# Kernel tuning notes

Hardware: AMD Instinct MI355X
Metric: run time of the kernel (lower is better)

## Reference

```python
import jax, jax.numpy as jnp
import numpy as np

N = 1_000_000
H = 256
DIMS = [1, H, H, H, H]
N_LAYERS = 4  # 4 linear layers, sin activation after the first 3


def setup_inputs() -> dict:
    key = jax.random.key(0)
    ks = jax.random.split(key, 1 + 2 * N_LAYERS)
    d = {"x": jax.random.normal(ks[0], (N, 2), dtype=jnp.float32)}
    i = 1
    for pre in ("x", "t"):
        for l in range(N_LAYERS):
            lim = 1.0 / np.sqrt(DIMS[l])  # torch.nn.Linear default init range
            d[f"{pre}W{l}"] = jax.random.uniform(
                ks[i], (DIMS[l], DIMS[l + 1]), dtype=jnp.float32, minval=-lim, maxval=lim)
            d[f"{pre}b{l}"] = jnp.zeros((DIMS[l + 1],), dtype=jnp.float32)
            i += 1
    return d


def _mlp(h, params):
    # params: list of (W, b); sin activation after all but the last layer
    n = len(params)
    for idx, (W, b) in enumerate(params):
        h = h @ W + b
        if idx < n - 1:
            h = jnp.sin(h)
    return h


def reference(x, xW0, xb0, xW1, xb1, xW2, xb2, xW3, xb3,
              tW0, tb0, tW1, tb1, tW2, tb2, tW3, tb3):
    x_params = [(xW0, xb0), (xW1, xb1), (xW2, xb2), (xW3, xb3)]
    t_params = [(tW0, tb0), (tW1, tb1), (tW2, tb2), (tW3, tb3)]
    nx = _mlp(x[:, 0:1], x_params)  # [N, H]
    nt = _mlp(x[:, 1:2], t_params)  # [N, H]
    # diag(A @ B.T) == rowwise dot product; avoids the O(N^2) matmul
    even = jnp.sum(nx[:, 0::2] * nt[:, 0::2], axis=-1)  # [N]
    odd = jnp.sum(nx[:, 1::2] * nt[:, 1::2], axis=-1)   # [N]
    return jnp.stack([even, odd], axis=-1)  # [N, 2]
```

## Files before the change

kernel.cpp:

```cpp
#include <hip/hip_runtime.h>


typedef _Float16 f16x8 __attribute__((ext_vector_type(8)));
typedef _Float16 f16x4 __attribute__((ext_vector_type(4)));
typedef float f32x4 __attribute__((ext_vector_type(4)));

__device__ __forceinline__ int hswz(int m, int kbyte) {
    return m * 512 + ((((kbyte >> 4) ^ (m & 7)) & 31) << 4) + (kbyte & 15);
}

__device__ __forceinline__ void barrier_lds() {
    asm volatile("s_waitcnt lgkmcnt(0)" ::: "memory");
    __builtin_amdgcn_s_barrier();
}

__global__ void prepack(const float* __restrict__ xW1, const float* __restrict__ xW2,
                        const float* __restrict__ xW3, const float* __restrict__ tW1,
                        const float* __restrict__ tW2, const float* __restrict__ tW3,
                        _Float16* __restrict__ dst)
{
    int g = blockIdx.x * 256 + threadIdx.x;
    int L = g >> 16;
    int r = g & 65535;
    int j    = r & 7;
    int ln   = (r >> 3) & 15;
    int quad = (r >> 7) & 3;
    int nhi  = (r >> 9) & 15;
    int ks   = (r >> 13) & 1;
    int c    = (r >> 14) & 3;
    const float* W;
    switch (L) {
        case 0: W = xW1; break;
        case 1: W = xW2; break;
        case 2: W = xW3; break;
        case 3: W = tW1; break;
        case 4: W = tW2; break;
        default: W = tW3; break;
    }
    int n = nhi * 16 + ln;
    int k = c * 64 + ks * 32 + quad * 8 + j;
    dst[g] = (_Float16)W[k * 256 + n];
}


__device__ __forceinline__ void layer0_scalar(
    float xv, const float* __restrict__ W0, const float* __restrict__ b0,
    _Float16* __restrict__ hb, int tid)
{
    int m = tid >> 2;
    int q = tid & 3;
#pragma unroll
    for (int g = 0; g < 8; ++g) {
        int n0 = g * 32 + q * 8;
        f16x8 hv;
#pragma unroll
        for (int e = 0; e < 8; ++e) {
            float z = fmaf(xv, W0[n0 + e], b0[n0 + e]);
            hv[e] = (_Float16)__sinf(z);
        }
        *(f16x8*)((char*)hb + hswz(m, n0 * 2)) = hv;
    }
}

template<int MODE>
__device__ __forceinline__ void gemm_phase(
    const _Float16* __restrict__ Wl,
    const _Float16* __restrict__ Wnext,
    const _Float16* __restrict__ rb,
    f32x4 acc[4][4], f16x8 afr[2][4],
    f32x4 wacc[4][4],
    const float* __restrict__ wbias,
    _Float16* __restrict__ wb_lds,
    float xv,
    const float* __restrict__ W0,
    const float* __restrict__ b0,
    int tid, int lane, int ln, int quad, int wave)
{
    f32x4 zero = {0.f, 0.f, 0.f, 0.f};
#pragma unroll
    for (int i = 0; i < 4; ++i)
#pragma unroll
        for (int j = 0; j < 4; ++j)
            acc[i][j] = zero;

    const _Float16* abase = Wl + wave * 2048 + lane * 8;

    f16x8 bfr[2][4];
#pragma unroll
    for (int j = 0; j < 4; ++j)
        bfr[0][j] = *(const f16x8*)((const char*)rb +
                                    hswz(16 * j + ln, quad * 16));

#pragma unroll
    for (int g = 0; g < 8; ++g) {
        if (g < 7) {
#pragma unroll
            for (int j = 0; j < 4; ++j)
                bfr[(g + 1) & 1][j] = *(const f16x8*)((const char*)rb +
                                 hswz(16 * j + ln, (g + 1) * 64 + quad * 16));
        }

        __builtin_amdgcn_s_setprio(1);
#pragma unroll
        for (int i = 0; i < 4; ++i)
#pragma unroll
            for (int j = 0; j < 4; ++j)
                acc[i][j] = __builtin_amdgcn_mfma_f32_16x16x32_f16(
                    afr[g & 1][i], bfr[g & 1][j], acc[i][j], 0, 0, 0);
        __builtin_amdgcn_s_setprio(0);

        if (g < 6) {
#pragma unroll
            for (int i = 0; i < 4; ++i)
                afr[g & 1][i] = *(const f16x8*)(abase + (g + 2) * 8192 + i * 512);
        } else if (Wnext) {
#pragma unroll
            for (int i = 0; i < 4; ++i)
                afr[g & 1][i] = *(const f16x8*)(Wnext + (g - 6) * 8192 +
                                                wave * 2048 + lane * 8 + i * 512);
        }

        if (MODE == 1) {
            const int wi = g >> 1;
            const int nb = wave * 64 + 16 * wi + quad * 4;
            f32x4 bv = *(const f32x4*)&wbias[nb];
#pragma unroll
            for (int jo = 0; jo < 2; ++jo) {
                const int wj = (g & 1) * 2 + jo;
                f16x4 hv;
                hv[0] = (_Float16)__sinf(wacc[wi][wj][0] + bv[0]);
                hv[1] = (_Float16)__sinf(wacc[wi][wj][1] + bv[1]);
                hv[2] = (_Float16)__sinf(wacc[wi][wj][2] + bv[2]);
                hv[3] = (_Float16)__sinf(wacc[wi][wj][3] + bv[3]);
                *(f16x4*)((char*)wb_lds + hswz(16 * wj + ln, nb * 2)) = hv;
            }
        } else if (MODE == 2) {
            const int m = tid >> 2, q = tid & 3;
            const int n0 = g * 32 + q * 8;
            f16x8 hv;
#pragma unroll
            for (int e = 0; e < 8; ++e) {
                float z = fmaf(xv, W0[n0 + e], b0[n0 + e]);
                hv[e] = (_Float16)__sinf(z);
            }
            *(f16x8*)((char*)wb_lds + hswz(m, n0 * 2)) = hv;
        }
    }
}

__global__ __launch_bounds__(256, 2)
void mlp_fused(const float* __restrict__ x,
               const float* __restrict__ xW0, const float* __restrict__ xb0,
               const float* __restrict__ xb1, const float* __restrict__ xb2,
               const float* __restrict__ xb3,
               const float* __restrict__ tW0, const float* __restrict__ tb0,
               const float* __restrict__ tb1, const float* __restrict__ tb2,
               const float* __restrict__ tb3,
               const _Float16* __restrict__ Wp,
               float* __restrict__ out)
{
    __shared__ __align__(16) _Float16 hbuf[2][64 * 256];
    __shared__ __align__(16) float    params[10 * 256];

    const int tid = threadIdx.x;
    const int lane = tid & 63;
    const int wave = tid >> 6;
    const int ln = lane & 15;
    const int quad = lane >> 4;
    const int row0 = blockIdx.x * 64;

    {
        const float* psrc[10] = {xW0, xb0, tW0, tb0, xb1, xb2, xb3, tb1, tb2, tb3};
#pragma unroll
        for (int s = 0; s < 10; ++s)
            params[s * 256 + tid] = psrc[s][tid];
    }
    const float2 xv2 = ((const float2*)x)[row0 + (tid >> 2)];

    f32x4 xacc[4][4], tacc[4][4];
    f16x8 afr[2][4];

#pragma unroll
    for (int s = 0; s < 2; ++s)
#pragma unroll
        for (int i = 0; i < 4; ++i)
            afr[s][i] = *(const f16x8*)(Wp + s * 8192 + wave * 2048 +
                                        lane * 8 + i * 512);
    barrier_lds();

    layer0_scalar(xv2.x, &params[0], &params[256], hbuf[0], tid);
    barrier_lds();

    gemm_phase<2>(Wp + 0 * 65536, Wp + 3 * 65536, hbuf[0], xacc, afr,
                  nullptr, nullptr, hbuf[1],
                  xv2.y, &params[2 * 256], &params[3 * 256],
                  tid, lane, ln, quad, wave);
    barrier_lds();
    gemm_phase<1>(Wp + 3 * 65536, Wp + 1 * 65536, hbuf[1], tacc, afr,
                  xacc, &params[4 * 256], hbuf[0],
                  0.f, nullptr, nullptr, tid, lane, ln, quad, wave);
    barrier_lds();
    gemm_phase<1>(Wp + 1 * 65536, Wp + 4 * 65536, hbuf[0], xacc, afr,
                  tacc, &params[7 * 256], hbuf[1],
                  0.f, nullptr, nullptr, tid, lane, ln, quad, wave);
    barrier_lds();
    gemm_phase<1>(Wp + 4 * 65536, Wp + 2 * 65536, hbuf[1], tacc, afr,
                  xacc, &params[5 * 256], hbuf[0],
                  0.f, nullptr, nullptr, tid, lane, ln, quad, wave);
    barrier_lds();
    gemm_phase<1>(Wp + 2 * 65536, Wp + 5 * 65536, hbuf[0], xacc, afr,
                  tacc, &params[8 * 256], hbuf[1],
                  0.f, nullptr, nullptr, tid, lane, ln, quad, wave);
    barrier_lds();
    gemm_phase<0>(Wp + 5 * 65536, nullptr, hbuf[1], tacc, afr,
                  nullptr, nullptr, nullptr,
                  0.f, nullptr, nullptr, tid, lane, ln, quad, wave);

    const float* xb3l = &params[6 * 256];
    const float* tb3l = &params[9 * 256];
    float ev[4] = {0.f, 0.f, 0.f, 0.f};
    float od[4] = {0.f, 0.f, 0.f, 0.f};
#pragma unroll
    for (int i = 0; i < 4; ++i) {
        int nb = wave * 64 + 16 * i + quad * 4;
        f32x4 xb = *(const f32x4*)&xb3l[nb];
        f32x4 tb = *(const f32x4*)&tb3l[nb];
#pragma unroll
        for (int j = 0; j < 4; ++j) {
            float a0 = xacc[i][j][0] + xb[0], c0 = tacc[i][j][0] + tb[0];
            float a1 = xacc[i][j][1] + xb[1], c1 = tacc[i][j][1] + tb[1];
            float a2 = xacc[i][j][2] + xb[2], c2 = tacc[i][j][2] + tb[2];
            float a3 = xacc[i][j][3] + xb[3], c3 = tacc[i][j][3] + tb[3];
            ev[j] += a0 * c0 + a2 * c2;
            od[j] += a1 * c1 + a3 * c3;
        }
    }
#pragma unroll
    for (int j = 0; j < 4; ++j) {
        ev[j] += __shfl_xor(ev[j], 16, 64);
        ev[j] += __shfl_xor(ev[j], 32, 64);
        od[j] += __shfl_xor(od[j], 16, 64);
        od[j] += __shfl_xor(od[j], 32, 64);
    }

    float* red = (float*)hbuf[0];
    if (lane < 16) {
#pragma unroll
        for (int j = 0; j < 4; ++j) {
            red[wave * 128 + j * 32 + lane * 2 + 0] = ev[j];
            red[wave * 128 + j * 32 + lane * 2 + 1] = od[j];
        }
    }
    __syncthreads();
    if (tid < 128) {
        int jj = tid >> 5, m16 = (tid >> 1) & 15, p = tid & 1;
        int base = jj * 32 + m16 * 2 + p;
        float s = red[base] + red[128 + base] + red[256 + base] + red[384 + base];
        out[(row0 + 16 * jj + m16) * 2 + p] = s;
    }
}

extern "C" void kernel_launch(void* const* d_in, const int* in_sizes, int n_in,
                              void* d_out, int out_size, void* d_ws, size_t ws_size,
                              hipStream_t stream)
{
    const float* x   = (const float*)d_in[0];
    const float* xW0 = (const float*)d_in[1];
    const float* xb0 = (const float*)d_in[2];
    const float* xW1 = (const float*)d_in[3];
    const float* xb1 = (const float*)d_in[4];
    const float* xW2 = (const float*)d_in[5];
    const float* xb2 = (const float*)d_in[6];
    const float* xW3 = (const float*)d_in[7];
    const float* xb3 = (const float*)d_in[8];
    const float* tW0 = (const float*)d_in[9];
    const float* tb0 = (const float*)d_in[10];
    const float* tW1 = (const float*)d_in[11];
    const float* tb1 = (const float*)d_in[12];
    const float* tW2 = (const float*)d_in[13];
    const float* tb2 = (const float*)d_in[14];
    const float* tW3 = (const float*)d_in[15];
    const float* tb3 = (const float*)d_in[16];

    _Float16* Wp = (_Float16*)d_ws;
    const int N = in_sizes[0] / 2;

    prepack<<<1536, 256, 0, stream>>>(xW1, xW2, xW3, tW1, tW2, tW3, Wp);
    mlp_fused<<<N / 64, 256, 0, stream>>>(x, xW0, xb0, xb1, xb2, xb3,
                                          tW0, tb0, tb1, tb2, tb3,
                                          Wp, (float*)d_out);
}
```

Measured before the change: 825.9 us.

## Switch fused MLP GEMMs from 16x16x32 to 32x32x16 MFMA tiles

Replaces the 16x16x32 f16 MFMA tiling with 32x32x16 MFMAs, so each wave holds a 2x2 grid of 32x32 accumulators instead of 4x4 16x16 ones. The weight prepack layout, the LDS swizzle (now XORing with the full row index), the B-fragment prefetch schedule, the sin/bias epilogue write-back and the final row reduction are all rewritten to match the new fragment layout. The larger MFMA shape is meant to cut instruction issue count and LDS B-fragment traffic per FLOP. In exchange it changes register pressure and the bank-conflict pattern of the LDS accesses.

```diff
diff --git a/kernel.cpp b/kernel.cpp
--- a/kernel.cpp
+++ b/kernel.cpp
@@ -4,9 +4,10 @@
 typedef _Float16 f16x8 __attribute__((ext_vector_type(8)));
 typedef _Float16 f16x4 __attribute__((ext_vector_type(4)));
 typedef float f32x4 __attribute__((ext_vector_type(4)));
-
-__device__ __forceinline__ int hswz(int m, int kbyte) {
-    return m * 512 + ((((kbyte >> 4) ^ (m & 7)) & 31) << 4) + (kbyte & 15);
+typedef float f32x16 __attribute__((ext_vector_type(16)));
+
+__device__ __forceinline__ int hswz32(int m, int kbyte) {
+    return m * 512 + ((((kbyte >> 4) ^ m) & 31) << 4) + (kbyte & 15);
 }
 
 __device__ __forceinline__ void barrier_lds() {
@@ -22,12 +23,12 @@
     int g = blockIdx.x * 256 + threadIdx.x;
     int L = g >> 16;
     int r = g & 65535;
-    int j    = r & 7;
-    int ln   = (r >> 3) & 15;
-    int quad = (r >> 7) & 3;
-    int nhi  = (r >> 9) & 15;
-    int ks   = (r >> 13) & 1;
-    int c    = (r >> 14) & 3;
+    int j  = r & 7;
+    int l  = (r >> 3) & 63;
+    int ks = (r >> 9) & 1;
+    int ci = (r >> 10) & 1;
+    int wv = (r >> 11) & 3;
+    int gg = (r >> 13) & 7;
     const float* W;
     switch (L) {
         case 0: W = xW1; break;
@@ -37,8 +38,8 @@
         case 4: W = tW2; break;
         default: W = tW3; break;
     }
-    int n = nhi * 16 + ln;
-    int k = c * 64 + ks * 32 + quad * 8 + j;
+    int n = wv * 64 + ci * 32 + (l & 31);
+    int k = gg * 32 + ks * 16 + ((l >> 5) & 1) * 8 + j;
     dst[g] = (_Float16)W[k * 256 + n];
 }
 
@@ -58,7 +59,7 @@
             float z = fmaf(xv, W0[n0 + e], b0[n0 + e]);
             hv[e] = (_Float16)__sinf(z);
         }
-        *(f16x8*)((char*)hb + hswz(m, n0 * 2)) = hv;
+        *(f16x8*)((char*)hb + hswz32(m, n0 * 2)) = hv;
     }
 }
 
@@ -67,72 +68,85 @@
     const _Float16* __restrict__ Wl,
     const _Float16* __restrict__ Wnext,
     const _Float16* __restrict__ rb,
-    f32x4 acc[4][4], f16x8 afr[2][4],
-    f32x4 wacc[4][4],
+    f32x16 acc[2][2], f16x8 afr[2][4],
+    f32x16 wacc[2][2],
     const float* __restrict__ wbias,
     _Float16* __restrict__ wb_lds,
     float xv,
     const float* __restrict__ W0,
     const float* __restrict__ b0,
-    int tid, int lane, int ln, int quad, int wave)
-{
-    f32x4 zero = {0.f, 0.f, 0.f, 0.f};
-#pragma unroll
-    for (int i = 0; i < 4; ++i)
-#pragma unroll
-        for (int j = 0; j < 4; ++j)
-            acc[i][j] = zero;
+    int tid, int lane, int wave)
+{
+    const int ml = lane & 31;
+    const int kh = lane >> 5;
+
+    f32x16 zero;
+#pragma unroll
+    for (int e = 0; e < 16; ++e) zero[e] = 0.f;
+#pragma unroll
+    for (int ci = 0; ci < 2; ++ci)
+#pragma unroll
+        for (int ri = 0; ri < 2; ++ri)
+            acc[ci][ri] = zero;
 
     const _Float16* abase = Wl + wave * 2048 + lane * 8;
 
     f16x8 bfr[2][4];
 #pragma unroll
-    for (int j = 0; j < 4; ++j)
-        bfr[0][j] = *(const f16x8*)((const char*)rb +
-                                    hswz(16 * j + ln, quad * 16));
+    for (int s = 0; s < 2; ++s)
+#pragma unroll
+        for (int ri = 0; ri < 2; ++ri)
+#pragma unroll
+            for (int ks = 0; ks < 2; ++ks)
+                bfr[s][ri * 2 + ks] = *(const f16x8*)((const char*)rb +
+                    hswz32(ri * 32 + ml, s * 64 + ks * 32 + kh * 16));
 
 #pragma unroll
     for (int g = 0; g < 8; ++g) {
-        if (g < 7) {
-#pragma unroll
-            for (int j = 0; j < 4; ++j)
-                bfr[(g + 1) & 1][j] = *(const f16x8*)((const char*)rb +
-                                 hswz(16 * j + ln, (g + 1) * 64 + quad * 16));
-        }
-
         __builtin_amdgcn_s_setprio(1);
 #pragma unroll
-        for (int i = 0; i < 4; ++i)
-#pragma unroll
-            for (int j = 0; j < 4; ++j)
-                acc[i][j] = __builtin_amdgcn_mfma_f32_16x16x32_f16(
-                    afr[g & 1][i], bfr[g & 1][j], acc[i][j], 0, 0, 0);
+        for (int ks = 0; ks < 2; ++ks)
+#pragma unroll
+            for (int ci = 0; ci < 2; ++ci)
+#pragma unroll
+                for (int ri = 0; ri < 2; ++ri)
+                    acc[ci][ri] = __builtin_amdgcn_mfma_f32_32x32x16_f16(
+                        afr[g & 1][ci * 2 + ks], bfr[g & 1][ri * 2 + ks],
+                        acc[ci][ri], 0, 0, 0);
         __builtin_amdgcn_s_setprio(0);
 
         if (g < 6) {
 #pragma unroll
-            for (int i = 0; i < 4; ++i)
-                afr[g & 1][i] = *(const f16x8*)(abase + (g + 2) * 8192 + i * 512);
+            for (int ri = 0; ri < 2; ++ri)
+#pragma unroll
+                for (int ks = 0; ks < 2; ++ks)
+                    bfr[g & 1][ri * 2 + ks] = *(const f16x8*)((const char*)rb +
+                        hswz32(ri * 32 + ml, (g + 2) * 64 + ks * 32 + kh * 16));
+        }
+        if (g < 6) {
+#pragma unroll
+            for (int f = 0; f < 4; ++f)
+                afr[g & 1][f] = *(const f16x8*)(abase + (g + 2) * 8192 + f * 512);
         } else if (Wnext) {
 #pragma unroll
-            for (int i = 0; i < 4; ++i)
-                afr[g & 1][i] = *(const f16x8*)(Wnext + (g - 6) * 8192 +
-                                                wave * 2048 + lane * 8 + i * 512);
+            for (int f = 0; f < 4; ++f)
+                afr[g & 1][f] = *(const f16x8*)(Wnext + (g - 6) * 8192 +
+                                                wave * 2048 + lane * 8 + f * 512);
         }
 
         if (MODE == 1) {
-            const int wi = g >> 1;
-            const int nb = wave * 64 + 16 * wi + quad * 4;
-            f32x4 bv = *(const f32x4*)&wbias[nb];
 #pragma unroll
             for (int jo = 0; jo < 2; ++jo) {
-                const int wj = (g & 1) * 2 + jo;
+                const int s  = g * 2 + jo;
+                const int ci = s >> 3, ri = (s >> 2) & 1, gq = s & 3;
+                const int nb = wave * 64 + ci * 32 + gq * 8 + 4 * kh;
+                f32x4 bv = *(const f32x4*)&wbias[nb];
                 f16x4 hv;
-                hv[0] = (_Float16)__sinf(wacc[wi][wj][0] + bv[0]);
-                hv[1] = (_Float16)__sinf(wacc[wi][wj][1] + bv[1]);
-                hv[2] = (_Float16)__sinf(wacc[wi][wj][2] + bv[2]);
-                hv[3] = (_Float16)__sinf(wacc[wi][wj][3] + bv[3]);
-                *(f16x4*)((char*)wb_lds + hswz(16 * wj + ln, nb * 2)) = hv;
+                hv[0] = (_Float16)__sinf(wacc[ci][ri][gq * 4 + 0] + bv[0]);
+                hv[1] = (_Float16)__sinf(wacc[ci][ri][gq * 4 + 1] + bv[1]);
+                hv[2] = (_Float16)__sinf(wacc[ci][ri][gq * 4 + 2] + bv[2]);
+                hv[3] = (_Float16)__sinf(wacc[ci][ri][gq * 4 + 3] + bv[3]);
+                *(f16x4*)((char*)wb_lds + hswz32(ri * 32 + ml, nb * 2)) = hv;
             }
         } else if (MODE == 2) {
             const int m = tid >> 2, q = tid & 3;
@@ -143,7 +157,7 @@
                 float z = fmaf(xv, W0[n0 + e], b0[n0 + e]);
                 hv[e] = (_Float16)__sinf(z);
             }
-            *(f16x8*)((char*)wb_lds + hswz(m, n0 * 2)) = hv;
+            *(f16x8*)((char*)wb_lds + hswz32(m, n0 * 2)) = hv;
         }
     }
 }
@@ -165,8 +179,8 @@
     const int tid = threadIdx.x;
     const int lane = tid & 63;
     const int wave = tid >> 6;
-    const int ln = lane & 15;
-    const int quad = lane >> 4;
+    const int ml = lane & 31;
+    const int kh = lane >> 5;
     const int row0 = blockIdx.x * 64;
 
     {
@@ -177,15 +191,15 @@
     }
     const float2 xv2 = ((const float2*)x)[row0 + (tid >> 2)];
 
-    f32x4 xacc[4][4], tacc[4][4];
+    f32x16 xacc[2][2], tacc[2][2];
     f16x8 afr[2][4];
 
 #pragma unroll
     for (int s = 0; s < 2; ++s)
 #pragma unroll
-        for (int i = 0; i < 4; ++i)
-            afr[s][i] = *(const f16x8*)(Wp + s * 8192 + wave * 2048 +
-                                        lane * 8 + i * 512);
+        for (int f = 0; f < 4; ++f)
+            afr[s][f] = *(const f16x8*)(Wp + s * 8192 + wave * 2048 +
+                                        lane * 8 + f * 512);
     barrier_lds();
 
     layer0_scalar(xv2.x, &params[0], &params[256], hbuf[0], tid);
@@ -193,70 +207,69 @@
 
     gemm_phase<2>(Wp + 0 * 65536, Wp + 3 * 65536, hbuf[0], xacc, afr,
                   nullptr, nullptr, hbuf[1],
-                  xv2.y, &params[2 * 256], &params[3 * 256],
-                  tid, lane, ln, quad, wave);
+                  xv2.y, &params[2 * 256], &params[3 * 256], tid, lane, wave);
     barrier_lds();
     gemm_phase<1>(Wp + 3 * 65536, Wp + 1 * 65536, hbuf[1], tacc, afr,
                   xacc, &params[4 * 256], hbuf[0],
-                  0.f, nullptr, nullptr, tid, lane, ln, quad, wave);
+                  0.f, nullptr, nullptr, tid, lane, wave);
     barrier_lds();
     gemm_phase<1>(Wp + 1 * 65536, Wp + 4 * 65536, hbuf[0], xacc, afr,
                   tacc, &params[7 * 256], hbuf[1],
-                  0.f, nullptr, nullptr, tid, lane, ln, quad, wave);
+                  0.f, nullptr, nullptr, tid, lane, wave);
     barrier_lds();
     gemm_phase<1>(Wp + 4 * 65536, Wp + 2 * 65536, hbuf[1], tacc, afr,
                   xacc, &params[5 * 256], hbuf[0],
-                  0.f, nullptr, nullptr, tid, lane, ln, quad, wave);
+                  0.f, nullptr, nullptr, tid, lane, wave);
     barrier_lds();
     gemm_phase<1>(Wp + 2 * 65536, Wp + 5 * 65536, hbuf[0], xacc, afr,
                   tacc, &params[8 * 256], hbuf[1],
-                  0.f, nullptr, nullptr, tid, lane, ln, quad, wave);
+                  0.f, nullptr, nullptr, tid, lane, wave);
     barrier_lds();
     gemm_phase<0>(Wp + 5 * 65536, nullptr, hbuf[1], tacc, afr,
                   nullptr, nullptr, nullptr,
-                  0.f, nullptr, nullptr, tid, lane, ln, quad, wave);
+                  0.f, nullptr, nullptr, tid, lane, wave);
 
     const float* xb3l = &params[6 * 256];
     const float* tb3l = &params[9 * 256];
-    float ev[4] = {0.f, 0.f, 0.f, 0.f};
-    float od[4] = {0.f, 0.f, 0.f, 0.f};
-#pragma unroll
-    for (int i = 0; i < 4; ++i) {
-        int nb = wave * 64 + 16 * i + quad * 4;
-        f32x4 xb = *(const f32x4*)&xb3l[nb];
-        f32x4 tb = *(const f32x4*)&tb3l[nb];
-#pragma unroll
-        for (int j = 0; j < 4; ++j) {
-            float a0 = xacc[i][j][0] + xb[0], c0 = tacc[i][j][0] + tb[0];
-            float a1 = xacc[i][j][1] + xb[1], c1 = tacc[i][j][1] + tb[1];
-            float a2 = xacc[i][j][2] + xb[2], c2 = tacc[i][j][2] + tb[2];
-            float a3 = xacc[i][j][3] + xb[3], c3 = tacc[i][j][3] + tb[3];
-            ev[j] += a0 * c0 + a2 * c2;
-            od[j] += a1 * c1 + a3 * c3;
-        }
-    }
-#pragma unroll
-    for (int j = 0; j < 4; ++j) {
-        ev[j] += __shfl_xor(ev[j], 16, 64);
-        ev[j] += __shfl_xor(ev[j], 32, 64);
-        od[j] += __shfl_xor(od[j], 16, 64);
-        od[j] += __shfl_xor(od[j], 32, 64);
+    float ev[2] = {0.f, 0.f};
+    float od[2] = {0.f, 0.f};
+#pragma unroll
+    for (int ci = 0; ci < 2; ++ci)
+#pragma unroll
+        for (int gq = 0; gq < 4; ++gq) {
+            int nb = wave * 64 + ci * 32 + gq * 8 + 4 * kh;
+            f32x4 xb = *(const f32x4*)&xb3l[nb];
+            f32x4 tb = *(const f32x4*)&tb3l[nb];
+#pragma unroll
+            for (int ri = 0; ri < 2; ++ri) {
+                float a0 = xacc[ci][ri][gq * 4 + 0] + xb[0], c0 = tacc[ci][ri][gq * 4 + 0] + tb[0];
+                float a1 = xacc[ci][ri][gq * 4 + 1] + xb[1], c1 = tacc[ci][ri][gq * 4 + 1] + tb[1];
+                float a2 = xacc[ci][ri][gq * 4 + 2] + xb[2], c2 = tacc[ci][ri][gq * 4 + 2] + tb[2];
+                float a3 = xacc[ci][ri][gq * 4 + 3] + xb[3], c3 = tacc[ci][ri][gq * 4 + 3] + tb[3];
+                ev[ri] += a0 * c0 + a2 * c2;
+                od[ri] += a1 * c1 + a3 * c3;
+            }
+        }
+#pragma unroll
+    for (int ri = 0; ri < 2; ++ri) {
+        ev[ri] += __shfl_xor(ev[ri], 32, 64);
+        od[ri] += __shfl_xor(od[ri], 32, 64);
     }
 
     float* red = (float*)hbuf[0];
-    if (lane < 16) {
-#pragma unroll
-        for (int j = 0; j < 4; ++j) {
-            red[wave * 128 + j * 32 + lane * 2 + 0] = ev[j];
-            red[wave * 128 + j * 32 + lane * 2 + 1] = od[j];
+    if (lane < 32) {
+#pragma unroll
+        for (int ri = 0; ri < 2; ++ri) {
+            red[wave * 128 + ri * 64 + ml * 2 + 0] = ev[ri];
+            red[wave * 128 + ri * 64 + ml * 2 + 1] = od[ri];
         }
     }
     __syncthreads();
     if (tid < 128) {
-        int jj = tid >> 5, m16 = (tid >> 1) & 15, p = tid & 1;
-        int base = jj * 32 + m16 * 2 + p;
+        int p = tid & 1, row = tid >> 1;
+        int base = (row >> 5) * 64 + (row & 31) * 2 + p;
         float s = red[base] + red[128 + base] + red[256 + base] + red[384 + base];
-        out[(row0 + 16 * jj + m16) * 2 + p] = s;
+        out[(row0 + row) * 2 + p] = s;
     }
 }
 
```

Result: slower. 955.8 us (+15.7%).

## Double block row tile to 128 rows with 8 waves each owning 32 output columns

Applied to the files above, without the earlier changes.

The fused MLP kernel now processes 128 rows per block with 512 threads (8 waves). Each wave computes a 32-column slice across all 128 rows, and the prepacked weight layout is reordered to match. Each weight fragment loaded from global memory now feeds twice as many rows, halving the global weight traffic per row. The cost is doubled LDS activation buffers (about 128KB plus params), which may limit occupancy, plus 8 B-fragment LDS reads per k-step instead of double-buffered 4. Bounds checks on N are added for a partial last block.

```diff
diff --git a/kernel.cpp b/kernel.cpp
--- a/kernel.cpp
+++ b/kernel.cpp
@@ -22,12 +22,11 @@
     int g = blockIdx.x * 256 + threadIdx.x;
     int L = g >> 16;
     int r = g & 65535;
-    int j    = r & 7;
-    int ln   = (r >> 3) & 15;
-    int quad = (r >> 7) & 3;
-    int nhi  = (r >> 9) & 15;
-    int ks   = (r >> 13) & 1;
-    int c    = (r >> 14) & 3;
+    int j  = r & 7;
+    int l  = (r >> 3) & 63;
+    int ci = (r >> 9) & 1;
+    int w  = (r >> 10) & 7;
+    int gg = (r >> 13) & 7;
     const float* W;
     switch (L) {
         case 0: W = xW1; break;
@@ -37,8 +36,8 @@
         case 4: W = tW2; break;
         default: W = tW3; break;
     }
-    int n = nhi * 16 + ln;
-    int k = c * 64 + ks * 32 + quad * 8 + j;
+    int n = w * 32 + ci * 16 + (l & 15);
+    int k = gg * 32 + ((l >> 4) & 3) * 8 + j;
     dst[g] = (_Float16)W[k * 256 + n];
 }
 
@@ -67,8 +66,8 @@
     const _Float16* __restrict__ Wl,
     const _Float16* __restrict__ Wnext,
     const _Float16* __restrict__ rb,
-    f32x4 acc[4][4], f16x8 afr[2][4],
-    f32x4 wacc[4][4],
+    f32x4 acc[2][8], f16x8 afr[2][2],
+    f32x4 wacc[2][8],
     const float* __restrict__ wbias,
     _Float16* __restrict__ wb_lds,
     float xv,
@@ -78,61 +77,60 @@
 {
     f32x4 zero = {0.f, 0.f, 0.f, 0.f};
 #pragma unroll
-    for (int i = 0; i < 4; ++i)
-#pragma unroll
-        for (int j = 0; j < 4; ++j)
-            acc[i][j] = zero;
-
-    const _Float16* abase = Wl + wave * 2048 + lane * 8;
-
-    f16x8 bfr[2][4];
-#pragma unroll
-    for (int j = 0; j < 4; ++j)
-        bfr[0][j] = *(const f16x8*)((const char*)rb +
-                                    hswz(16 * j + ln, quad * 16));
+    for (int ci = 0; ci < 2; ++ci)
+#pragma unroll
+        for (int ri = 0; ri < 8; ++ri)
+            acc[ci][ri] = zero;
+
+    const _Float16* abase = Wl + wave * 1024 + lane * 8;
+
+    f16x8 bfr[8];
+#pragma unroll
+    for (int ri = 0; ri < 8; ++ri)
+        bfr[ri] = *(const f16x8*)((const char*)rb +
+                                  hswz(16 * ri + ln, quad * 16));
 
 #pragma unroll
     for (int g = 0; g < 8; ++g) {
+        __builtin_amdgcn_s_setprio(1);
+#pragma unroll
+        for (int ci = 0; ci < 2; ++ci)
+#pragma unroll
+            for (int ri = 0; ri < 8; ++ri)
+                acc[ci][ri] = __builtin_amdgcn_mfma_f32_16x16x32_f16(
+                    afr[g & 1][ci], bfr[ri], acc[ci][ri], 0, 0, 0);
+        __builtin_amdgcn_s_setprio(0);
+
         if (g < 7) {
 #pragma unroll
-            for (int j = 0; j < 4; ++j)
-                bfr[(g + 1) & 1][j] = *(const f16x8*)((const char*)rb +
-                                 hswz(16 * j + ln, (g + 1) * 64 + quad * 16));
-        }
-
-        __builtin_amdgcn_s_setprio(1);
-#pragma unroll
-        for (int i = 0; i < 4; ++i)
-#pragma unroll
-            for (int j = 0; j < 4; ++j)
-                acc[i][j] = __builtin_amdgcn_mfma_f32_16x16x32_f16(
-                    afr[g & 1][i], bfr[g & 1][j], acc[i][j], 0, 0, 0);
-        __builtin_amdgcn_s_setprio(0);
-
+            for (int ri = 0; ri < 8; ++ri)
+                bfr[ri] = *(const f16x8*)((const char*)rb +
+                              hswz(16 * ri + ln, (g + 1) * 64 + quad * 16));
+        }
         if (g < 6) {
 #pragma unroll
-            for (int i = 0; i < 4; ++i)
-                afr[g & 1][i] = *(const f16x8*)(abase + (g + 2) * 8192 + i * 512);
+            for (int ci = 0; ci < 2; ++ci)
+                afr[g & 1][ci] = *(const f16x8*)(abase + (g + 2) * 8192 + ci * 512);
         } else if (Wnext) {
 #pragma unroll
-            for (int i = 0; i < 4; ++i)
-                afr[g & 1][i] = *(const f16x8*)(Wnext + (g - 6) * 8192 +
-                                                wave * 2048 + lane * 8 + i * 512);
+            for (int ci = 0; ci < 2; ++ci)
+                afr[g & 1][ci] = *(const f16x8*)(Wnext + (g - 6) * 8192 +
+                                                 wave * 1024 + lane * 8 + ci * 512);
         }
 
         if (MODE == 1) {
-            const int wi = g >> 1;
-            const int nb = wave * 64 + 16 * wi + quad * 4;
-            f32x4 bv = *(const f32x4*)&wbias[nb];
 #pragma unroll
             for (int jo = 0; jo < 2; ++jo) {
-                const int wj = (g & 1) * 2 + jo;
+                const int s  = g * 2 + jo;
+                const int cw = s >> 3, rw = s & 7;
+                const int nb = wave * 32 + cw * 16 + quad * 4;
+                f32x4 bv = *(const f32x4*)&wbias[nb];
                 f16x4 hv;
-                hv[0] = (_Float16)__sinf(wacc[wi][wj][0] + bv[0]);
-                hv[1] = (_Float16)__sinf(wacc[wi][wj][1] + bv[1]);
-                hv[2] = (_Float16)__sinf(wacc[wi][wj][2] + bv[2]);
-                hv[3] = (_Float16)__sinf(wacc[wi][wj][3] + bv[3]);
-                *(f16x4*)((char*)wb_lds + hswz(16 * wj + ln, nb * 2)) = hv;
+                hv[0] = (_Float16)__sinf(wacc[cw][rw][0] + bv[0]);
+                hv[1] = (_Float16)__sinf(wacc[cw][rw][1] + bv[1]);
+                hv[2] = (_Float16)__sinf(wacc[cw][rw][2] + bv[2]);
+                hv[3] = (_Float16)__sinf(wacc[cw][rw][3] + bv[3]);
+                *(f16x4*)((char*)wb_lds + hswz(16 * rw + ln, nb * 2)) = hv;
             }
         } else if (MODE == 2) {
             const int m = tid >> 2, q = tid & 3;
@@ -148,7 +146,7 @@
     }
 }
 
-__global__ __launch_bounds__(256, 2)
+__global__ __launch_bounds__(512, 2)
 void mlp_fused(const float* __restrict__ x,
                const float* __restrict__ xW0, const float* __restrict__ xb0,
                const float* __restrict__ xb1, const float* __restrict__ xb2,
@@ -157,9 +155,9 @@
                const float* __restrict__ tb1, const float* __restrict__ tb2,
                const float* __restrict__ tb3,
                const _Float16* __restrict__ Wp,
-               float* __restrict__ out)
-{
-    __shared__ __align__(16) _Float16 hbuf[2][64 * 256];
+               float* __restrict__ out, int N)
+{
+    __shared__ __align__(16) _Float16 hbuf[2][128 * 256];
     __shared__ __align__(16) float    params[10 * 256];
 
     const int tid = threadIdx.x;
@@ -167,25 +165,28 @@
     const int wave = tid >> 6;
     const int ln = lane & 15;
     const int quad = lane >> 4;
-    const int row0 = blockIdx.x * 64;
+    const int row0 = blockIdx.x * 128;
 
     {
         const float* psrc[10] = {xW0, xb0, tW0, tb0, xb1, xb2, xb3, tb1, tb2, tb3};
-#pragma unroll
-        for (int s = 0; s < 10; ++s)
-            params[s * 256 + tid] = psrc[s][tid];
-    }
-    const float2 xv2 = ((const float2*)x)[row0 + (tid >> 2)];
-
-    f32x4 xacc[4][4], tacc[4][4];
-    f16x8 afr[2][4];
+        int half = tid >> 8, e = tid & 255;
+#pragma unroll
+        for (int s = 0; s < 5; ++s)
+            params[(half * 5 + s) * 256 + e] = psrc[half * 5 + s][e];
+    }
+    const int myrow = row0 + (tid >> 2);
+    const float2 xv2 = (myrow < N) ? ((const float2*)x)[myrow]
+                                   : make_float2(0.f, 0.f);
+
+    f32x4 xacc[2][8], tacc[2][8];
+    f16x8 afr[2][2];
 
 #pragma unroll
     for (int s = 0; s < 2; ++s)
 #pragma unroll
-        for (int i = 0; i < 4; ++i)
-            afr[s][i] = *(const f16x8*)(Wp + s * 8192 + wave * 2048 +
-                                        lane * 8 + i * 512);
+        for (int ci = 0; ci < 2; ++ci)
+            afr[s][ci] = *(const f16x8*)(Wp + s * 8192 + wave * 1024 +
+                                         lane * 8 + ci * 512);
     barrier_lds();
 
     layer0_scalar(xv2.x, &params[0], &params[256], hbuf[0], tid);
@@ -218,45 +219,50 @@
 
     const float* xb3l = &params[6 * 256];
     const float* tb3l = &params[9 * 256];
-    float ev[4] = {0.f, 0.f, 0.f, 0.f};
-    float od[4] = {0.f, 0.f, 0.f, 0.f};
-#pragma unroll
-    for (int i = 0; i < 4; ++i) {
-        int nb = wave * 64 + 16 * i + quad * 4;
+    float ev[8], od[8];
+#pragma unroll
+    for (int ri = 0; ri < 8; ++ri) { ev[ri] = 0.f; od[ri] = 0.f; }
+#pragma unroll
+    for (int ci = 0; ci < 2; ++ci) {
+        int nb = wave * 32 + ci * 16 + quad * 4;
         f32x4 xb = *(const f32x4*)&xb3l[nb];
         f32x4 tb = *(const f32x4*)&tb3l[nb];
 #pragma unroll
-        for (int j = 0; j < 4; ++j) {
-            float a0 = xacc[i][j][0] + xb[0], c0 = tacc[i][j][0] + tb[0];
-            float a1 = xacc[i][j][1] + xb[1], c1 = tacc[i][j][1] + tb[1];
-            float a2 = xacc[i][j][2] + xb[2], c2 = tacc[i][j][2] + tb[2];
-            float a3 = xacc[i][j][3] + xb[3], c3 = tacc[i][j][3] + tb[3];
-            ev[j] += a0 * c0 + a2 * c2;
-            od[j] += a1 * c1 + a3 * c3;
-        }
-    }
-#pragma unroll
-    for (int j = 0; j < 4; ++j) {
-        ev[j] += __shfl_xor(ev[j], 16, 64);
-        ev[j] += __shfl_xor(ev[j], 32, 64);
-        od[j] += __shfl_xor(od[j], 16, 64);
-        od[j] += __shfl_xor(od[j], 32, 64);
+        for (int ri = 0; ri < 8; ++ri) {
+            float a0 = xacc[ci][ri][0] + xb[0], c0 = tacc[ci][ri][0] + tb[0];
+            float a1 = xacc[ci][ri][1] + xb[1], c1 = tacc[ci][ri][1] + tb[1];
+            float a2 = xacc[ci][ri][2] + xb[2], c2 = tacc[ci][ri][2] + tb[2];
+            float a3 = xacc[ci][ri][3] + xb[3], c3 = tacc[ci][ri][3] + tb[3];
+            ev[ri] += a0 * c0 + a2 * c2;
+            od[ri] += a1 * c1 + a3 * c3;
+        }
+    }
+#pragma unroll
+    for (int ri = 0; ri < 8; ++ri) {
+        ev[ri] += __shfl_xor(ev[ri], 16, 64);
+        ev[ri] += __shfl_xor(ev[ri], 32, 64);
+        od[ri] += __shfl_xor(od[ri], 16, 64);
+        od[ri] += __shfl_xor(od[ri], 32, 64);
     }
 
     float* red = (float*)hbuf[0];
     if (lane < 16) {
 #pragma unroll
-        for (int j = 0; j < 4; ++j) {
-            red[wave * 128 + j * 32 + lane * 2 + 0] = ev[j];
-            red[wave * 128 + j * 32 + lane * 2 + 1] = od[j];
+        for (int ri = 0; ri < 8; ++ri) {
+            red[wave * 256 + ri * 32 + ln * 2 + 0] = ev[ri];
+            red[wave * 256 + ri * 32 + ln * 2 + 1] = od[ri];
         }
     }
     __syncthreads();
-    if (tid < 128) {
-        int jj = tid >> 5, m16 = (tid >> 1) & 15, p = tid & 1;
-        int base = jj * 32 + m16 * 2 + p;
-        float s = red[base] + red[128 + base] + red[256 + base] + red[384 + base];
-        out[(row0 + 16 * jj + m16) * 2 + p] = s;
+    if (tid < 256) {
+        int p = tid & 1, row = tid >> 1;
+        int base = (row >> 4) * 32 + (row & 15) * 2 + p;
+        float s = 0.f;
+#pragma unroll
+        for (int w = 0; w < 8; ++w)
+            s += red[w * 256 + base];
+        if (row0 + row < N)
+            out[(row0 + row) * 2 + p] = s;
     }
 }
 
@@ -284,9 +290,10 @@
 
     _Float16* Wp = (_Float16*)d_ws;
     const int N = in_sizes[0] / 2;
+    const int nblk = (N + 127) / 128;
 
     prepack<<<1536, 256, 0, stream>>>(xW1, xW2, xW3, tW1, tW2, tW3, Wp);
-    mlp_fused<<<N / 64, 256, 0, stream>>>(x, xW0, xb0, xb1, xb2, xb3,
-                                          tW0, tb0, tb1, tb2, tb3,
-                                          Wp, (float*)d_out);
-}
+    mlp_fused<<<nblk, 512, 0, stream>>>(x, xW0, xb0, xb1, xb2, xb3,
+                                        tW0, tb0, tb1, tb2, tb3,
+                                        Wp, (float*)d_out, N);
+}
```

Result: slower. 865.0 us (+4.7%).
